# Optimization experiments

Hardware: AMD Instinct MI355X
Metric: run time of the kernel (lower is better)

## Reference

```python
import jax, jax.numpy as jnp
import numpy as np
from jax import lax

DRUG_LEN = 150
PROT_LEN = 1000
CHAR_DIM = 64
CONV = 40
C4 = CONV * 4  # 160
PROT_OUT = PROT_LEN - (4 - 1) - (8 - 1) - (12 - 1)  # 979


def conv1d(x, w, b):
    # x: (B, Cin, L), w: (Cout, Cin, K) -> (B, Cout, L-K+1), VALID
    y = lax.conv_general_dilated(x, w, window_strides=(1,), padding='VALID',
                                 dimension_numbers=('NCH', 'OIH', 'NCH'))
    return y + b[None, :, None]


def setup_inputs() -> dict:
    key = jax.random.key(0)
    ks = jax.random.split(key, 24)
    B = 4
    drug = jax.random.normal(ks[0], (B, DRUG_LEN, C4), dtype=jnp.float32)
    num_atoms = jax.random.randint(ks[1], (B,), 1, DRUG_LEN + 1)
    protein = jax.random.randint(ks[2], (B, PROT_LEN), 0, 26)

    def lin(k, dout, din, scale=None):
        s = scale if scale is not None else 1.0 / np.sqrt(din)
        kw, kb = jax.random.split(k)
        W = jax.random.uniform(kw, (dout, din), jnp.float32, -s, s)
        b = jax.random.uniform(kb, (dout,), jnp.float32, -s, s)
        return W, b

    protein_embed = jax.random.normal(ks[3], (26, CHAR_DIM), dtype=jnp.float32)
    protein_embed = protein_embed.at[0].set(0.0)  # padding_idx=0

    def conv_w(k, cout, cin, ksz):
        s = 1.0 / np.sqrt(cin * ksz)
        kw, kb = jax.random.split(k)
        w = jax.random.uniform(kw, (cout, cin, ksz), jnp.float32, -s, s)
        b = jax.random.uniform(kb, (cout,), jnp.float32, -s, s)
        return w, b

    w1, b1 = conv_w(ks[4], CONV, CHAR_DIM, 4)
    w2, b2 = conv_w(ks[5], CONV * 2, CONV, 8)
    w3, b3 = conv_w(ks[6], C4, CONV * 2, 12)
    Wd, bd = lin(ks[7], C4, C4)
    Wp, bp = lin(ks[8], C4, C4)
    Watt, batt = lin(ks[9], C4, C4)
    W1, bf1 = lin(ks[10], 1024, C4 * 2)
    W2, bf2 = lin(ks[11], 1024, 1024)
    W3, bf3 = lin(ks[12], 512, 1024)
    Wo, bo = lin(ks[13], 2, 512)
    return dict(drug=drug, num_atoms=num_atoms, protein=protein,
                protein_embed=protein_embed, w1=w1, b1=b1, w2=w2, b2=b2,
                w3=w3, b3=b3, Wd=Wd, bd=bd, Wp=Wp, bp=bp, Watt=Watt,
                batt=batt, W1=W1, bf1=bf1, W2=W2, bf2=bf2, W3=W3, bf3=bf3,
                Wo=Wo, bo=bo)


def _forward(drug, num_atoms, protein, protein_embed, w1, b1, w2, b2, w3, b3,
             Wd, bd, Wp, bp, Watt, batt, W1, bf1, W2, bf2, W3, bf3, Wo, bo):
    relu = jax.nn.relu
    drugConv = jnp.transpose(drug, (0, 2, 1))                 # (B,160,150)
    pe = jnp.transpose(protein_embed[protein], (0, 2, 1))     # (B,64,1000)
    h = relu(conv1d(pe, w1, b1))
    h = relu(conv1d(h, w2, b2))
    proteinConv = relu(conv1d(h, w3, b3))                     # (B,160,979)

    drug_att = drug @ Wd.T + bd                               # (B,150,160)
    dmask = (jnp.arange(DRUG_LEN)[None, :] < num_atoms[:, None])
    drug_att = drug_att * dmask[:, :, None]
    protein_att = jnp.transpose(proteinConv, (0, 2, 1)) @ Wp.T + bp  # (B,979,160)
    pmask = (protein > 0)[:, :PROT_OUT]
    protein_att = protein_att * pmask[:, :, None]

    # Broadcast outer-sum + relu; Linear commutes with mean (affine), so apply
    # attention_layer after reducing, identical math to Linear-then-mean.
    R = relu(drug_att[:, :, None, :] + protein_att[:, None, :, :])  # (B,150,979,160)
    Cmean = jnp.mean(R, axis=2)  # (B,150,160)
    Pmean = jnp.mean(R, axis=1)  # (B,979,160)
    Compound_atte = jax.nn.sigmoid(Cmean @ Watt.T + batt)  # (B,150,160)
    Protein_atte = jax.nn.sigmoid(Pmean @ Watt.T + batt)   # (B,979,160)

    drugConv = drugConv * (0.5 + jnp.transpose(Compound_atte, (0, 2, 1)))
    proteinConv = proteinConv * (0.5 + jnp.transpose(Protein_atte, (0, 2, 1)))
    d = jnp.max(drugConv, axis=2)      # (B,160) max-pool over full length
    p = jnp.max(proteinConv, axis=2)   # (B,160)
    pair = jnp.concatenate([d, p], axis=1)  # (B,320)

    lrelu = lambda x: jax.nn.leaky_relu(x, 0.01)
    f1 = lrelu(pair @ W1.T + bf1)
    f2 = lrelu(f1 @ W2.T + bf2)
    f3 = lrelu(f2 @ W3.T + bf3)
    return f3 @ Wo.T + bo  # (B,2)


def reference(drug, num_atoms, protein, protein_embed, w1, b1, w2, b2, w3, b3,
              Wd, bd, Wp, bp, Watt, batt, W1, bf1, W2, bf2, W3, bf3, Wo, bo):
    return _forward(drug, num_atoms, protein, protein_embed, w1, b1, w2, b2,
                    w3, b3, Wd, bd, Wp, bp, Watt, batt, W1, bf1, W2, bf2,
                    W3, bf3, Wo, bo)
```

## Files before the change

kernel.cpp:

```cpp
#include <hip/hip_runtime.h>
#include <math.h>

#define BB 4
#define DL 150
#define PL 1000
#define CD 64
#define NC1 40
#define NC2 80
#define NC3 160
#define L1O 997
#define L2O 990
#define L3O 979
#define L1P 1000
#define L2P 992
#define L3P 980
#define DLP 152
#define PLP 984
#define JP 992
#define NINF (-1e30f)

typedef __attribute__((ext_vector_type(8))) short bf16x8;
typedef __attribute__((ext_vector_type(4))) float f32x4;

__device__ __forceinline__ float relu_(float x){ return fmaxf(x, 0.f); }
__device__ __forceinline__ float lrelu_(float x){ return x > 0.f ? x : 0.01f * x; }

__device__ __forceinline__ unsigned fenc(float x){
  unsigned u = __float_as_uint(x);
  return (u & 0x80000000u) ? ~u : (u | 0x80000000u);
}
__device__ __forceinline__ float fdec(unsigned u){
  return __uint_as_float((u & 0x80000000u) ? (u & 0x7fffffffu) : ~u);
}
__device__ __forceinline__ float4 relu4_(float4 v){
  v.x = fmaxf(v.x, 0.f); v.y = fmaxf(v.y, 0.f);
  v.z = fmaxf(v.z, 0.f); v.w = fmaxf(v.w, 0.f);
  return v;
}
__device__ __forceinline__ unsigned short bf16_(float x){
  unsigned u = __float_as_uint(x);
  unsigned r = (u + 0x7FFFu + ((u >> 16) & 1u)) >> 16;
  return (unsigned short)r;
}

__device__ __forceinline__ f32x4 mfma_k160(const unsigned short* __restrict__ Wb,
                                           const unsigned short* __restrict__ Xb,
                                           int co0, int j0, int lane){
  int col = lane & 15, g = lane >> 4;
  f32x4 acc = {0.f, 0.f, 0.f, 0.f};
  const unsigned short* wr = Wb + (size_t)(co0 + col) * 160 + g * 8;
  const unsigned short* xr = Xb + (size_t)(j0 + col) * 160 + g * 8;
  #pragma unroll
  for (int k0 = 0; k0 < 5; k0++){
    bf16x8 av = *(const bf16x8*)(wr + k0 * 32);
    bf16x8 bv = *(const bf16x8*)(xr + k0 * 32);
    acc = __builtin_amdgcn_mfma_f32_16x16x32_bf16(av, bv, acc, 0, 0, 0);
  }
  return acc;
}

__global__ __launch_bounds__(256) void k_prep(const float* __restrict__ emb,
                       const float* __restrict__ w1, float* __restrict__ projG,
                       const float* __restrict__ w3, unsigned short* __restrict__ w3r,
                       const float* __restrict__ Wp, unsigned short* __restrict__ Wpb,
                       const float* __restrict__ Watt, unsigned short* __restrict__ Wattb){
  int blk = blockIdx.x;
  if (blk < 17){
    int e = blk * 256 + threadIdx.x;
    if (e >= 26 * 160) return;
    int tok = e / 160, rem = e % 160, k = rem / 40, co = rem % 40;
    float a = 0.f;
    const float* er = emb + tok * CD;
    const float* wr = w1 + co * (CD * 4) + k;
    #pragma unroll 8
    for (int ci = 0; ci < CD; ci++) a = fmaf(er[ci], wr[ci * 4], a);
    projG[tok * 161 + k * 40 + co] = a;
    return;
  }
  if (blk < 737){
    int e = (blk - 17) * 256 + threadIdx.x;
    if (e >= 12 * 160 * 96) return;
    int kk = e / (160 * 96); int r = e % (160 * 96);
    int co = r / 96, ci = r % 96;
    float v = (ci < NC2) ? w3[(size_t)co * 960 + ci * 12 + kk] : 0.f;
    w3r[e] = bf16_(v);
    return;
  }
  if (blk < 837){
    int e = (blk - 737) * 256 + threadIdx.x;
    if (e < 160 * 160) Wpb[e] = bf16_(Wp[e]);
    return;
  }
  int e = (blk - 837) * 256 + threadIdx.x;
  if (e < 160 * 160) Wattb[e] = bf16_(Watt[e]);
}

__global__ __launch_bounds__(256) void k_conv1(const int* __restrict__ prot,
                        const float* __restrict__ projG, const float* __restrict__ b1,
                        float* __restrict__ h1){
  __shared__ float sp[26 * 161];
  int b = blockIdx.x / 80;
  int t = (blockIdx.x % 80) * 256 + threadIdx.x;
  for (int k = threadIdx.x; k < 26 * 161; k += 256) sp[k] = projG[k];
  __syncthreads();
  int p = t & 1023, co2 = t >> 10;
  if (p >= L1O) return;
  const int* pr = prot + b * PL + p;
  int t0 = pr[0], t1 = pr[1], t2 = pr[2], t3 = pr[3];
  #pragma unroll
  for (int c = 0; c < 2; c++){
    int co = co2 * 2 + c;
    float a = b1[co] + sp[t0 * 161 + co] + sp[t1 * 161 + 40 + co]
            + sp[t2 * 161 + 80 + co] + sp[t3 * 161 + 120 + co];
    h1[(size_t)(b * NC1 + co) * L1P + p] = relu_(a);
  }
}

#define C2XW 44
#define C2WP 324
__global__ __launch_bounds__(128) void k_c2(const float* __restrict__ h1,
                        const float* __restrict__ w, const float* __restrict__ bias,
                        float* __restrict__ h2){
  __shared__ float xs[NC1 * C2XW];
  __shared__ float wl[16 * C2WP];
  int blk = blockIdx.x;
  int pt = blk % 31; int t = blk / 31;
  int cog = t % 5; int b = t / 5;
  int co0 = cog * 16, pblk = pt * 32;
  int tid = threadIdx.x;
  const float* xb = h1 + (size_t)(b * NC1) * L1P + pblk;
  for (int i = tid; i < 440; i += 128){
    int r = i / 11, c = i % 11;
    *(float4*)(&xs[r * C2XW + c * 4]) = *(const float4*)(xb + (size_t)r * L1P + c * 4);
  }
  for (int i = tid; i < 1280; i += 128){
    int cc = i / 80, c = i % 80;
    *(float4*)(&wl[cc * C2WP + c * 4]) =
        *(const float4*)(w + (size_t)(co0 + cc) * 320 + c * 4);
  }
  __syncthreads();
  int co_l = tid >> 3, pg = tid & 7, p0 = pg * 4;
  float acc[4] = {0,0,0,0};
  const float* wc = &wl[co_l * C2WP];
  #pragma unroll 2
  for (int ci = 0; ci < NC1; ci++){
    const float* xrow = &xs[ci * C2XW + p0];
    float xv[12];
    *(float4*)(&xv[0]) = *(const float4*)(xrow);
    *(float4*)(&xv[4]) = *(const float4*)(xrow + 4);
    *(float4*)(&xv[8]) = *(const float4*)(xrow + 8);
    float wk[8];
    *(float4*)(&wk[0]) = *(const float4*)(wc + ci * 8);
    *(float4*)(&wk[4]) = *(const float4*)(wc + ci * 8 + 4);
    #pragma unroll
    for (int k = 0; k < 8; k++){
      #pragma unroll
      for (int pp = 0; pp < 4; pp++)
        acc[pp] = fmaf(xv[pp + k], wk[k], acc[pp]);
    }
  }
  int co = co0 + co_l;
  float bv = bias[co];
  int pbase = pblk + p0;
  float* yr = h2 + (size_t)(b * NC2 + co) * L2P + pbase;
  if (pbase + 3 < L2O){
    float4 o; o.x = relu_(acc[0] + bv); o.y = relu_(acc[1] + bv);
    o.z = relu_(acc[2] + bv); o.w = relu_(acc[3] + bv);
    *(float4*)yr = o;
  } else {
    #pragma unroll
    for (int pp = 0; pp < 4; pp++)
      if (pbase + pp < L2O) yr[pp] = relu_(acc[pp] + bv);
  }
}

__global__ __launch_bounds__(256) void k_t2(const float* __restrict__ h2,
                        unsigned short* __restrict__ h2bT){
  __shared__ float tile[32][33];
  int blk = blockIdx.x;
  int pt = blk % 31; int t = blk / 31;
  int cit = t % 3; int b = t / 3;
  int ci0 = cit * 32, p0 = pt * 32;
  int r = threadIdx.x >> 5, c = threadIdx.x & 31;
  #pragma unroll
  for (int rr = 0; rr < 4; rr++){
    int ci = ci0 + r * 4 + rr;
    float v = (ci < NC2) ? h2[(size_t)(b * NC2 + ci) * L2P + p0 + c] : 0.f;
    tile[r * 4 + rr][c] = v;
  }
  __syncthreads();
  #pragma unroll
  for (int rr = 0; rr < 4; rr++){
    int prow = p0 + r * 4 + rr;
    h2bT[((size_t)b * 992 + prow) * 96 + ci0 + c] = bf16_(tile[c][r * 4 + rr]);
  }
}

__global__ __launch_bounds__(256) void k_c3m(const unsigned short* __restrict__ h2bT,
                        const unsigned short* __restrict__ w3r,
                        const float* __restrict__ bias, float* __restrict__ pconv,
                        unsigned short* __restrict__ pconvTb){
  int blk = blockIdx.x;
  int pt = blk % 16; int t = blk / 16;
  int cog = t % 10; int b = t / 10;
  int co0 = cog * 16;
  int wave = threadIdx.x >> 6, lane = threadIdx.x & 63;
  int col = lane & 15, g = lane >> 4;
  int p0 = pt * 64 + wave * 16;
  f32x4 acc = {0.f, 0.f, 0.f, 0.f};
  const unsigned short* wbase = w3r + (size_t)(co0 + col) * 96 + g * 8;
  const unsigned short* xbase = h2bT + (size_t)b * 992 * 96 + g * 8;
  int prow = p0 + col;
  for (int kk = 0; kk < 12; kk++){
    int rp = prow + kk; if (rp > 991) rp = 991;
    const unsigned short* xr = xbase + (size_t)rp * 96;
    const unsigned short* wr = wbase + (size_t)kk * (160 * 96);
    #pragma unroll
    for (int ks = 0; ks < 3; ks++){
      bf16x8 av = *(const bf16x8*)(wr + ks * 32);
      bf16x8 bv = *(const bf16x8*)(xr + ks * 32);
      acc = __builtin_amdgcn_mfma_f32_16x16x32_bf16(av, bv, acc, 0, 0, 0);
    }
  }
  if (p0 >= L3O) return;
  int p = p0 + col;
  if (p < L3O){
    unsigned short tb[4];
    #pragma unroll
    for (int r = 0; r < 4; r++){
      int co = co0 + g * 4 + r;
      float v = acc[r] + bias[co];
      pconv[(size_t)(b * NC3 + co) * L3P + p] = v;
      tb[r] = bf16_(relu_(v));
    }
    *(uint2*)(&pconvTb[((size_t)b * JP + p) * 160 + co0 + g * 4]) = *(uint2*)tb;
  }
}

__global__ __launch_bounds__(256) void k_patt(const float* __restrict__ drug,
                        const int* __restrict__ natoms,
                        const float* __restrict__ Wd, const float* __restrict__ bd,
                        float* __restrict__ dattT, unsigned* __restrict__ enc,
                        const unsigned short* __restrict__ pconvTb,
                        const int* __restrict__ prot,
                        const unsigned short* __restrict__ Wpb,
                        const float* __restrict__ bp, float* __restrict__ pattT){
  int blk = blockIdx.x;
  int tid = threadIdx.x;
  if (blk < 160){
    if (blk == 0){
      for (int k = tid; k < 2 * BB * NC3; k += 256) enc[k] = 0u;
    }
    int b = blk / 40, c0 = (blk % 40) * 4;
    int i = tid;
    if (i >= DL) return;
    const float4* xr = (const float4*)(drug + ((size_t)b * DL + i) * NC3);
    float4 a[4];
    #pragma unroll
    for (int cc = 0; cc < 4; cc++) a[cc] = make_float4(0.f, 0.f, 0.f, 0.f);
    for (int k4 = 0; k4 < 40; k4++){
      float4 xv = xr[k4];
      #pragma unroll
      for (int cc = 0; cc < 4; cc++){
        float4 wv = ((const float4*)(Wd + (size_t)(c0 + cc) * NC3))[k4];
        a[cc].x = fmaf(xv.x, wv.x, a[cc].x);
        a[cc].y = fmaf(xv.y, wv.y, a[cc].y);
        a[cc].z = fmaf(xv.z, wv.z, a[cc].z);
        a[cc].w = fmaf(xv.w, wv.w, a[cc].w);
      }
    }
    bool act = i < natoms[b];
    #pragma unroll
    for (int cc = 0; cc < 4; cc++){
      float r = act ? (a[cc].x + a[cc].y + a[cc].z + a[cc].w + bd[c0 + cc]) : 0.f;
      dattT[(size_t)(b * NC3 + c0 + cc) * DLP + i] = r;
    }
    return;
  }
  int q = blk - 160;
  int jt = q % 62, b = q / 62;
  int j0 = jt * 16;
  int wave = tid >> 6, lane = tid & 63;
  int col = lane & 15, g = lane >> 4;
  const unsigned short* Xb = pconvTb + (size_t)b * JP * 160;
  for (int ct = wave; ct < 10; ct += 4){
    int co0 = ct * 16;
    f32x4 acc = mfma_k160(Wpb, Xb, co0, j0, lane);
    int j = j0 + col;
    if (j < L3O){
      bool act = prot[b * PL + j] > 0;
      #pragma unroll
      for (int r = 0; r < 4; r++){
        int co = co0 + g * 4 + r;
        pattT[(size_t)(b * NC3 + co) * PLP + j] = act ? (acc[r] + bp[co]) : 0.f;
      }
    }
  }
}

__global__ __launch_bounds__(256) void k_means(const float* __restrict__ dattT,
                        const float* __restrict__ pattT,
                        float* __restrict__ cmeanT, float* __restrict__ pmeanT,
                        unsigned short* __restrict__ pmeanTb){
  __shared__ __align__(16) float sda[DLP];
  __shared__ __align__(16) float spa[PLP];
  __shared__ float scm[4][DLP];
  int b = blockIdx.x / NC3, c = blockIdx.x % NC3;
  int tid = threadIdx.x;
  const float4* dr = (const float4*)(dattT + (size_t)(b * NC3 + c) * DLP);
  const float4* pr = (const float4*)(pattT + (size_t)(b * NC3 + c) * PLP);
  if (tid < DLP / 4) *(float4*)(&sda[tid * 4]) = dr[tid];
  if (tid < PLP / 4) *(float4*)(&spa[tid * 4]) = pr[tid];
  __syncthreads();
  for (int t = tid; t < 600; t += 256){
    int i = t >> 2, qq = t & 3;
    int js = qq * 244;
    int je = (qq == 3) ? L3O : js + 244;
    float v = sda[i];
    float s0 = 0.f, s1 = 0.f, s2 = 0.f, s3 = 0.f;
    const float4* p4 = (const float4*)(spa + js);
    int n4 = (je - js) >> 2;
    for (int u = 0; u < n4; u++){
      float4 p = p4[u];
      s0 += relu_(v + p.x); s1 += relu_(v + p.y);
      s2 += relu_(v + p.z); s3 += relu_(v + p.w);
    }
    for (int j = js + n4 * 4; j < je; j++) s0 += relu_(v + spa[j]);
    scm[qq][i] = (s0 + s1) + (s2 + s3);
  }
  for (int j = tid; j < L3O; j += 256){
    float v = spa[j];
    float s0 = 0.f, s1 = 0.f, s2 = 0.f, s3 = 0.f;
    const float4* d4 = (const float4*)sda;
    #pragma unroll 4
    for (int u = 0; u < 37; u++){
      float4 d = d4[u];
      s0 += relu_(v + d.x); s1 += relu_(v + d.y);
      s2 += relu_(v + d.z); s3 += relu_(v + d.w);
    }
    s0 += relu_(v + sda[148]); s1 += relu_(v + sda[149]);
    float pm = ((s0 + s1) + (s2 + s3)) * (1.f / DL);
    pmeanT[(size_t)(b * NC3 + c) * PLP + j] = pm;
    pmeanTb[((size_t)b * JP + j) * 160 + c] = bf16_(pm);
  }
  __syncthreads();
  if (tid < DL){
    float s = (scm[0][tid] + scm[1][tid]) + (scm[2][tid] + scm[3][tid]);
    cmeanT[(size_t)(b * NC3 + c) * DLP + tid] = s * (1.f / L3O);
  }
}

__global__ __launch_bounds__(256) void k_atte(const float* __restrict__ cmeanT,
                        const unsigned short* __restrict__ pmeanTb,
                        const float* __restrict__ Watt,
                        const unsigned short* __restrict__ Wattb,
                        const float* __restrict__ batt,
                        const float* __restrict__ drug,
                        const float* __restrict__ pconv, unsigned* __restrict__ enc){
  int blk = blockIdx.x;
  int tid = threadIdx.x;
  if (blk < 160){
    __shared__ float sred[4][4];
    int b = blk / 40, c0 = (blk % 40) * 4;
    float m[4];
    #pragma unroll
    for (int cc = 0; cc < 4; cc++) m[cc] = NINF;
    int i = tid;
    if (i < DL){
      float acc[4];
      #pragma unroll
      for (int cc = 0; cc < 4; cc++) acc[cc] = batt[c0 + cc];
      const float* xc = cmeanT + (size_t)b * NC3 * DLP + i;
      const float* wr = Watt + (size_t)c0 * NC3;
      for (int cb = 0; cb < NC3; cb += 32){
        float xv[32];
        #pragma unroll
        for (int u = 0; u < 32; u++) xv[u] = xc[(size_t)(cb + u) * DLP];
        #pragma unroll
        for (int u = 0; u < 32; u++){
          #pragma unroll
          for (int cc = 0; cc < 4; cc++)
            acc[cc] = fmaf(xv[u], wr[(size_t)cc * NC3 + cb + u], acc[cc]);
        }
      }
      const float* gr = drug + ((size_t)b * DL + i) * NC3 + c0;
      #pragma unroll
      for (int cc = 0; cc < 4; cc++){
        float atte = 1.f / (1.f + expf(-acc[cc]));
        m[cc] = gr[cc] * (0.5f + atte);
      }
    }
    int wave = tid >> 6, lane = tid & 63;
    #pragma unroll
    for (int cc = 0; cc < 4; cc++){
      float v = m[cc];
      for (int off = 1; off < 64; off <<= 1) v = fmaxf(v, __shfl_xor(v, off, 64));
      if (lane == 0) sred[wave][cc] = v;
    }
    __syncthreads();
    if (tid < 4){
      float v = fmaxf(fmaxf(sred[0][tid], sred[1][tid]),
                      fmaxf(sred[2][tid], sred[3][tid]));
      atomicMax(&enc[b * NC3 + c0 + tid], fenc(v));
    }
    return;
  }
  int q = blk - 160;
  int jt = q % 62, b = q / 62;
  int j0 = jt * 16;
  int wave = tid >> 6, lane = tid & 63;
  int col = lane & 15, g = lane >> 4;
  const unsigned short* Xb = pmeanTb + (size_t)b * JP * 160;
  for (int ct = wave; ct < 10; ct += 4){
    int co0 = ct * 16;
    f32x4 acc = mfma_k160(Wattb, Xb, co0, j0, lane);
    int j = j0 + col;
    float m[4];
    #pragma unroll
    for (int r = 0; r < 4; r++){
      int co = co0 + g * 4 + r;
      if (j < L3O){
        float gate = 1.f / (1.f + expf(-(acc[r] + batt[co])));
        float pv = relu_(pconv[(size_t)(b * NC3 + co) * L3P + j]);
        m[r] = pv * (0.5f + gate);
      } else m[r] = NINF;
    }
    #pragma unroll
    for (int r = 0; r < 4; r++){
      #pragma unroll
      for (int off = 1; off < 16; off <<= 1)
        m[r] = fmaxf(m[r], __shfl_xor(m[r], off, 64));
    }
    if (col == 0){
      #pragma unroll
      for (int r = 0; r < 4; r++)
        atomicMax(&enc[BB * NC3 + b * NC3 + co0 + g * 4 + r], fenc(m[r]));
    }
  }
}

__global__ __launch_bounds__(256) void k_mlp1(const unsigned* __restrict__ enc,
                        const float* __restrict__ W1, const float* __restrict__ bf1,
                        float* __restrict__ f1){
  int b = blockIdx.x >> 6, og = blockIdx.x & 63;
  int o = og * 16 + (threadIdx.x >> 4);
  int q = threadIdx.x & 15;
  const float4* wr = (const float4*)(W1 + (size_t)o * 320);
  float4 a = make_float4(0.f, 0.f, 0.f, 0.f);
  #pragma unroll
  for (int mi = 0; mi < 5; mi++){
    int k4 = q + mi * 16;
    int k = k4 * 4;
    const unsigned* e = (k < 160) ? (enc + b * NC3 + k)
                                  : (enc + BB * NC3 + b * NC3 + (k - 160));
    float4 wv = wr[k4];
    a.x = fmaf(fdec(e[0]), wv.x, a.x);
    a.y = fmaf(fdec(e[1]), wv.y, a.y);
    a.z = fmaf(fdec(e[2]), wv.z, a.z);
    a.w = fmaf(fdec(e[3]), wv.w, a.w);
  }
  float r = a.x + a.y + a.z + a.w;
  r += __shfl_xor(r, 1, 64); r += __shfl_xor(r, 2, 64);
  r += __shfl_xor(r, 4, 64); r += __shfl_xor(r, 8, 64);
  if (q == 0) f1[b * 1024 + o] = lrelu_(r + bf1[o]);
}

__global__ __launch_bounds__(256) void k_mlp2(const float* __restrict__ x,
                        const float* __restrict__ W, const float* __restrict__ bias,
                        float* __restrict__ y){
  int b = blockIdx.x >> 6, og = blockIdx.x & 63;
  int o = og * 16 + (threadIdx.x >> 4);
  int q = threadIdx.x & 15;
  const float4* wr = (const float4*)(W + (size_t)o * 1024);
  const float4* xr = (const float4*)(x + b * 1024);
  float4 a = make_float4(0.f, 0.f, 0.f, 0.f);
  #pragma unroll
  for (int mi = 0; mi < 16; mi++){
    int k4 = q + mi * 16;
    float4 wv = wr[k4], xv = xr[k4];
    a.x = fmaf(xv.x, wv.x, a.x);
    a.y = fmaf(xv.y, wv.y, a.y);
    a.z = fmaf(xv.z, wv.z, a.z);
    a.w = fmaf(xv.w, wv.w, a.w);
  }
  float r = a.x + a.y + a.z + a.w;
  r += __shfl_xor(r, 1, 64); r += __shfl_xor(r, 2, 64);
  r += __shfl_xor(r, 4, 64); r += __shfl_xor(r, 8, 64);
  if (q == 0) y[b * 1024 + o] = lrelu_(r + bias[o]);
}

__global__ __launch_bounds__(256) void k_mlp3(const float* __restrict__ x,
                        const float* __restrict__ W, const float* __restrict__ bias,
                        float* __restrict__ y){
  int b = blockIdx.x >> 5, og = blockIdx.x & 31;
  int o = og * 16 + (threadIdx.x >> 4);
  int q = threadIdx.x & 15;
  const float4* wr = (const float4*)(W + (size_t)o * 1024);
  const float4* xr = (const float4*)(x + b * 1024);
  float4 a = make_float4(0.f, 0.f, 0.f, 0.f);
  #pragma unroll
  for (int mi = 0; mi < 16; mi++){
    int k4 = q + mi * 16;
    float4 wv = wr[k4], xv = xr[k4];
    a.x = fmaf(xv.x, wv.x, a.x);
    a.y = fmaf(xv.y, wv.y, a.y);
    a.z = fmaf(xv.z, wv.z, a.z);
    a.w = fmaf(xv.w, wv.w, a.w);
  }
  float r = a.x + a.y + a.z + a.w;
  r += __shfl_xor(r, 1, 64); r += __shfl_xor(r, 2, 64);
  r += __shfl_xor(r, 4, 64); r += __shfl_xor(r, 8, 64);
  if (q == 0) y[b * 512 + o] = lrelu_(r + bias[o]);
}

__global__ void k_mlp4(const float* __restrict__ f3, const float* __restrict__ Wo,
                       const float* __restrict__ bo, float* __restrict__ out){
  int tid = threadIdx.x;
  int g = tid >> 5, lane = tid & 31;
  int b = g >> 1, o = g & 1;
  const float4* xr = (const float4*)(f3 + b * 512);
  const float4* wr = (const float4*)(Wo + o * 512);
  float4 a = make_float4(0.f, 0.f, 0.f, 0.f);
  #pragma unroll
  for (int mI = 0; mI < 4; mI++){
    int k4 = lane + mI * 32;
    float4 xv = xr[k4], wv = wr[k4];
    a.x = fmaf(xv.x, wv.x, a.x);
    a.y = fmaf(xv.y, wv.y, a.y);
    a.z = fmaf(xv.z, wv.z, a.z);
    a.w = fmaf(xv.w, wv.w, a.w);
  }
  float r = a.x + a.y + a.z + a.w;
  for (int off = 16; off; off >>= 1) r += __shfl_xor(r, off, 64);
  if (lane == 0) out[b * 2 + o] = r + bo[o];
}

extern "C" void kernel_launch(void* const* d_in, const int* in_sizes, int n_in,
                              void* d_out, int out_size, void* d_ws, size_t ws_size,
                              hipStream_t stream) {
  const float* drug  = (const float*)d_in[0];
  const int*   natoms= (const int*)d_in[1];
  const int*   prot  = (const int*)d_in[2];
  const float* emb   = (const float*)d_in[3];
  const float* w1    = (const float*)d_in[4];
  const float* b1    = (const float*)d_in[5];
  const float* w2    = (const float*)d_in[6];
  const float* b2    = (const float*)d_in[7];
  const float* w3    = (const float*)d_in[8];
  const float* b3    = (const float*)d_in[9];
  const float* Wd    = (const float*)d_in[10];
  const float* bd    = (const float*)d_in[11];
  const float* Wp    = (const float*)d_in[12];
  const float* bp    = (const float*)d_in[13];
  const float* Watt  = (const float*)d_in[14];
  const float* batt  = (const float*)d_in[15];
  const float* W1    = (const float*)d_in[16];
  const float* bf1   = (const float*)d_in[17];
  const float* W2    = (const float*)d_in[18];
  const float* bf2   = (const float*)d_in[19];
  const float* W3    = (const float*)d_in[20];
  const float* bf3   = (const float*)d_in[21];
  const float* Wo    = (const float*)d_in[22];
  const float* bo    = (const float*)d_in[23];
  float* out = (float*)d_out;

  float* ws = (float*)d_ws;
  float* h1     = ws;
  float* cmeanT = ws;
  float* f1     = ws + 97280;
  float* f2     = ws + 101376;
  float* f3     = ws + 105472;
  float* h2     = ws + 160000;
  float* pconv  = ws + 477440;
  float* dattT  = ws + 1104640;
  float* pattT  = ws + 1201920;
  float* pmeanT = ws + 1831680;
  unsigned* enc = (unsigned*)(ws + 2461440);
  float* projG  = ws + 2461760;
  unsigned short* h2bT = (unsigned short*)(ws + 2466048);
  unsigned short* w3r  = (unsigned short*)(ws + 2656512);
  unsigned short* pconvTb = (unsigned short*)(ws + 2748672);
  unsigned short* pmeanTb = (unsigned short*)(ws + 3066112);
  unsigned short* Wpb   = (unsigned short*)(ws + 3383552);
  unsigned short* Wattb = (unsigned short*)(ws + 3396352);

  k_prep  <<<937, 256, 0, stream>>>(emb, w1, projG, w3, w3r, Wp, Wpb, Watt, Wattb);
  k_conv1 <<<BB * 80, 256, 0, stream>>>(prot, projG, b1, h1);
  k_c2    <<<620, 128, 0, stream>>>(h1, w2, b2, h2);
  k_t2    <<<372, 256, 0, stream>>>(h2, h2bT);
  k_c3m   <<<640, 256, 0, stream>>>(h2bT, w3r, b3, pconv, pconvTb);
  k_patt  <<<408, 256, 0, stream>>>(drug, natoms, Wd, bd, dattT, enc,
                                    pconvTb, prot, Wpb, bp, pattT);
  k_means <<<BB * NC3, 256, 0, stream>>>(dattT, pattT, cmeanT, pmeanT, pmeanTb);
  k_atte  <<<408, 256, 0, stream>>>(cmeanT, pmeanTb, Watt, Wattb, batt, drug,
                                    pconv, enc);
  k_mlp1  <<<256, 256, 0, stream>>>(enc, W1, bf1, f1);
  k_mlp2  <<<256, 256, 0, stream>>>(f1, W2, bf2, f2);
  k_mlp3  <<<128, 256, 0, stream>>>(f2, W3, bf3, f3);
  k_mlp4  <<<1, 256, 0, stream>>>(f3, Wo, bo, out);
}
```

Baseline: 106.2 us.

## Move conv2, drug linear and compound attention onto bf16 MFMA

Conv1 now writes a transposed bf16 activation, and conv2 becomes an MFMA kernel that writes the bf16 transposed layout conv3 consumes directly. This removes the separate transpose kernel and the fp32 intermediate. The drug projection and compound-side attention linear also switch from scalar fp32 FMA loops to MFMA, using new bf16 weight and drug copies made in the prep kernel. One launch and several fp32 round trips are removed, but more work shifts into the prep kernel and precision drops to bf16 on these paths.

```diff
diff --git a/kernel.cpp b/kernel.cpp
--- a/kernel.cpp
+++ b/kernel.cpp
@@ -11,8 +11,6 @@
 #define L1O 997
 #define L2O 990
 #define L3O 979
-#define L1P 1000
-#define L2P 992
 #define L3P 980
 #define DLP 152
 #define PLP 984
@@ -31,11 +29,6 @@
 }
 __device__ __forceinline__ float fdec(unsigned u){
   return __uint_as_float((u & 0x80000000u) ? (u & 0x7fffffffu) : ~u);
-}
-__device__ __forceinline__ float4 relu4_(float4 v){
-  v.x = fmaxf(v.x, 0.f); v.y = fmaxf(v.y, 0.f);
-  v.z = fmaxf(v.z, 0.f); v.w = fmaxf(v.w, 0.f);
-  return v;
 }
 __device__ __forceinline__ unsigned short bf16_(float x){
   unsigned u = __float_as_uint(x);
@@ -63,7 +56,10 @@
                        const float* __restrict__ w1, float* __restrict__ projG,
                        const float* __restrict__ w3, unsigned short* __restrict__ w3r,
                        const float* __restrict__ Wp, unsigned short* __restrict__ Wpb,
-                       const float* __restrict__ Watt, unsigned short* __restrict__ Wattb){
+                       const float* __restrict__ Watt, unsigned short* __restrict__ Wattb,
+                       const float* __restrict__ Wd, unsigned short* __restrict__ Wdb,
+                       const float* __restrict__ w2, unsigned short* __restrict__ w2r,
+                       const float* __restrict__ drug, unsigned short* __restrict__ drugb){
   int blk = blockIdx.x;
   if (blk < 17){
     int e = blk * 256 + threadIdx.x;
@@ -79,7 +75,6 @@
   }
   if (blk < 737){
     int e = (blk - 17) * 256 + threadIdx.x;
-    if (e >= 12 * 160 * 96) return;
     int kk = e / (160 * 96); int r = e % (160 * 96);
     int co = r / 96, ci = r % 96;
     float v = (ci < NC2) ? w3[(size_t)co * 960 + ci * 12 + kk] : 0.f;
@@ -88,111 +83,101 @@
   }
   if (blk < 837){
     int e = (blk - 737) * 256 + threadIdx.x;
-    if (e < 160 * 160) Wpb[e] = bf16_(Wp[e]);
-    return;
-  }
-  int e = (blk - 837) * 256 + threadIdx.x;
-  if (e < 160 * 160) Wattb[e] = bf16_(Watt[e]);
+    Wpb[e] = bf16_(Wp[e]);
+    return;
+  }
+  if (blk < 937){
+    int e = (blk - 837) * 256 + threadIdx.x;
+    Wattb[e] = bf16_(Watt[e]);
+    return;
+  }
+  if (blk < 1037){
+    int e = (blk - 937) * 256 + threadIdx.x;
+    Wdb[e] = bf16_(Wd[e]);
+    return;
+  }
+  if (blk < 1197){
+    int e = (blk - 1037) * 256 + threadIdx.x;
+    int kk = e / (80 * 64); int r = e % (80 * 64);
+    int co = r / 64, ci = r % 64;
+    float v = (ci < NC1) ? w2[(size_t)(co * NC1 + ci) * 8 + kk] : 0.f;
+    w2r[e] = bf16_(v);
+    return;
+  }
+  {
+    int e = (blk - 1197) * 256 + threadIdx.x;
+    int b = e / 25600; int r = e % 25600;
+    int i = r / 160, c = r % 160;
+    float v = (i < DL) ? drug[((size_t)b * DL + i) * 160 + c] : 0.f;
+    drugb[e] = bf16_(v);
+  }
 }
 
 __global__ __launch_bounds__(256) void k_conv1(const int* __restrict__ prot,
                         const float* __restrict__ projG, const float* __restrict__ b1,
-                        float* __restrict__ h1){
+                        unsigned short* __restrict__ h1bT){
   __shared__ float sp[26 * 161];
-  int b = blockIdx.x / 80;
-  int t = (blockIdx.x % 80) * 256 + threadIdx.x;
+  int b = blockIdx.x / 125;
+  int t = (blockIdx.x % 125) * 256 + threadIdx.x;
   for (int k = threadIdx.x; k < 26 * 161; k += 256) sp[k] = projG[k];
   __syncthreads();
-  int p = t & 1023, co2 = t >> 10;
-  if (p >= L1O) return;
-  const int* pr = prot + b * PL + p;
-  int t0 = pr[0], t1 = pr[1], t2 = pr[2], t3 = pr[3];
-  #pragma unroll
-  for (int c = 0; c < 2; c++){
-    int co = co2 * 2 + c;
-    float a = b1[co] + sp[t0 * 161 + co] + sp[t1 * 161 + 40 + co]
-            + sp[t2 * 161 + 80 + co] + sp[t3 * 161 + 120 + co];
-    h1[(size_t)(b * NC1 + co) * L1P + p] = relu_(a);
-  }
-}
-
-#define C2XW 44
-#define C2WP 324
-__global__ __launch_bounds__(128) void k_c2(const float* __restrict__ h1,
-                        const float* __restrict__ w, const float* __restrict__ bias,
-                        float* __restrict__ h2){
-  __shared__ float xs[NC1 * C2XW];
-  __shared__ float wl[16 * C2WP];
+  int ci = (t & 31) * 2, p = t >> 5;
+  float v0 = 0.f, v1 = 0.f;
+  if (p < L1O && ci < NC1){
+    const int* pr = prot + b * PL + p;
+    int t0 = pr[0], t1 = pr[1], t2 = pr[2], t3 = pr[3];
+    v0 = relu_(b1[ci] + sp[t0 * 161 + ci] + sp[t1 * 161 + 40 + ci]
+             + sp[t2 * 161 + 80 + ci] + sp[t3 * 161 + 120 + ci]);
+    int c1 = ci + 1;
+    v1 = relu_(b1[c1] + sp[t0 * 161 + c1] + sp[t1 * 161 + 40 + c1]
+             + sp[t2 * 161 + 80 + c1] + sp[t3 * 161 + 120 + c1]);
+  }
+  ushort2 o; o.x = bf16_(v0); o.y = bf16_(v1);
+  *(ushort2*)(&h1bT[((size_t)b * 1000 + p) * 64 + ci]) = o;
+}
+
+__global__ __launch_bounds__(256) void k_c2m(const unsigned short* __restrict__ h1bT,
+                        const unsigned short* __restrict__ w2r,
+                        const float* __restrict__ bias,
+                        unsigned short* __restrict__ h2bT){
   int blk = blockIdx.x;
-  int pt = blk % 31; int t = blk / 31;
+  int pt = blk % 16; int t = blk / 16;
   int cog = t % 5; int b = t / 5;
-  int co0 = cog * 16, pblk = pt * 32;
-  int tid = threadIdx.x;
-  const float* xb = h1 + (size_t)(b * NC1) * L1P + pblk;
-  for (int i = tid; i < 440; i += 128){
-    int r = i / 11, c = i % 11;
-    *(float4*)(&xs[r * C2XW + c * 4]) = *(const float4*)(xb + (size_t)r * L1P + c * 4);
-  }
-  for (int i = tid; i < 1280; i += 128){
-    int cc = i / 80, c = i % 80;
-    *(float4*)(&wl[cc * C2WP + c * 4]) =
-        *(const float4*)(w + (size_t)(co0 + cc) * 320 + c * 4);
-  }
-  __syncthreads();
-  int co_l = tid >> 3, pg = tid & 7, p0 = pg * 4;
-  float acc[4] = {0,0,0,0};
-  const float* wc = &wl[co_l * C2WP];
+  int co0 = cog * 16;
+  int wave = threadIdx.x >> 6, lane = threadIdx.x & 63;
+  int col = lane & 15, g = lane >> 4;
+  int p0 = pt * 64 + wave * 16;
+  if (p0 >= JP) return;
+  f32x4 acc = {0.f, 0.f, 0.f, 0.f};
+  const unsigned short* wbase = w2r + (size_t)(co0 + col) * 64 + g * 8;
+  const unsigned short* xbase = h1bT + (size_t)b * 1000 * 64 + g * 8;
+  int prow = p0 + col;
   #pragma unroll 2
-  for (int ci = 0; ci < NC1; ci++){
-    const float* xrow = &xs[ci * C2XW + p0];
-    float xv[12];
-    *(float4*)(&xv[0]) = *(const float4*)(xrow);
-    *(float4*)(&xv[4]) = *(const float4*)(xrow + 4);
-    *(float4*)(&xv[8]) = *(const float4*)(xrow + 8);
-    float wk[8];
-    *(float4*)(&wk[0]) = *(const float4*)(wc + ci * 8);
-    *(float4*)(&wk[4]) = *(const float4*)(wc + ci * 8 + 4);
-    #pragma unroll
-    for (int k = 0; k < 8; k++){
-      #pragma unroll
-      for (int pp = 0; pp < 4; pp++)
-        acc[pp] = fmaf(xv[pp + k], wk[k], acc[pp]);
-    }
-  }
-  int co = co0 + co_l;
-  float bv = bias[co];
-  int pbase = pblk + p0;
-  float* yr = h2 + (size_t)(b * NC2 + co) * L2P + pbase;
-  if (pbase + 3 < L2O){
-    float4 o; o.x = relu_(acc[0] + bv); o.y = relu_(acc[1] + bv);
-    o.z = relu_(acc[2] + bv); o.w = relu_(acc[3] + bv);
-    *(float4*)yr = o;
-  } else {
-    #pragma unroll
-    for (int pp = 0; pp < 4; pp++)
-      if (pbase + pp < L2O) yr[pp] = relu_(acc[pp] + bv);
-  }
-}
-
-__global__ __launch_bounds__(256) void k_t2(const float* __restrict__ h2,
-                        unsigned short* __restrict__ h2bT){
-  __shared__ float tile[32][33];
-  int blk = blockIdx.x;
-  int pt = blk % 31; int t = blk / 31;
-  int cit = t % 3; int b = t / 3;
-  int ci0 = cit * 32, p0 = pt * 32;
-  int r = threadIdx.x >> 5, c = threadIdx.x & 31;
-  #pragma unroll
-  for (int rr = 0; rr < 4; rr++){
-    int ci = ci0 + r * 4 + rr;
-    float v = (ci < NC2) ? h2[(size_t)(b * NC2 + ci) * L2P + p0 + c] : 0.f;
-    tile[r * 4 + rr][c] = v;
-  }
-  __syncthreads();
-  #pragma unroll
-  for (int rr = 0; rr < 4; rr++){
-    int prow = p0 + r * 4 + rr;
-    h2bT[((size_t)b * 992 + prow) * 96 + ci0 + c] = bf16_(tile[c][r * 4 + rr]);
+  for (int kk = 0; kk < 8; kk++){
+    int rp = prow + kk; if (rp > 999) rp = 999;
+    const unsigned short* xr = xbase + (size_t)rp * 64;
+    const unsigned short* wr = wbase + (size_t)kk * (80 * 64);
+    #pragma unroll
+    for (int ks = 0; ks < 2; ks++){
+      bf16x8 av = *(const bf16x8*)(wr + ks * 32);
+      bf16x8 bv = *(const bf16x8*)(xr + ks * 32);
+      acc = __builtin_amdgcn_mfma_f32_16x16x32_bf16(av, bv, acc, 0, 0, 0);
+    }
+  }
+  int p = p0 + col;
+  if (p < JP){
+    unsigned short tb[4];
+    bool live = p < L2O;
+    #pragma unroll
+    for (int r = 0; r < 4; r++){
+      int co = co0 + g * 4 + r;
+      tb[r] = live ? bf16_(relu_(acc[r] + bias[co])) : (unsigned short)0;
+    }
+    *(uint2*)(&h2bT[((size_t)b * JP + p) * 96 + co0 + g * 4]) = *(uint2*)tb;
+    if (cog == 4){
+      uint2 z = {0u, 0u};
+      *(uint2*)(&h2bT[((size_t)b * JP + p) * 96 + 80 + g * 4]) = z;
+    }
   }
 }
 
@@ -209,7 +194,7 @@
   int p0 = pt * 64 + wave * 16;
   f32x4 acc = {0.f, 0.f, 0.f, 0.f};
   const unsigned short* wbase = w3r + (size_t)(co0 + col) * 96 + g * 8;
-  const unsigned short* xbase = h2bT + (size_t)b * 992 * 96 + g * 8;
+  const unsigned short* xbase = h2bT + (size_t)b * JP * 96 + g * 8;
   int prow = p0 + col;
   for (int kk = 0; kk < 12; kk++){
     int rp = prow + kk; if (rp > 991) rp = 991;
@@ -237,9 +222,10 @@
   }
 }
 
-__global__ __launch_bounds__(256) void k_patt(const float* __restrict__ drug,
+__global__ __launch_bounds__(256) void k_pattm(const unsigned short* __restrict__ drugb,
                         const int* __restrict__ natoms,
-                        const float* __restrict__ Wd, const float* __restrict__ bd,
+                        const unsigned short* __restrict__ Wdb,
+                        const float* __restrict__ bd,
                         float* __restrict__ dattT, unsigned* __restrict__ enc,
                         const unsigned short* __restrict__ pconvTb,
                         const int* __restrict__ prot,
@@ -247,41 +233,33 @@
                         const float* __restrict__ bp, float* __restrict__ pattT){
   int blk = blockIdx.x;
   int tid = threadIdx.x;
-  if (blk < 160){
+  int wave = tid >> 6, lane = tid & 63;
+  int col = lane & 15, g = lane >> 4;
+  if (blk < 40){
     if (blk == 0){
       for (int k = tid; k < 2 * BB * NC3; k += 256) enc[k] = 0u;
     }
-    int b = blk / 40, c0 = (blk % 40) * 4;
-    int i = tid;
-    if (i >= DL) return;
-    const float4* xr = (const float4*)(drug + ((size_t)b * DL + i) * NC3);
-    float4 a[4];
-    #pragma unroll
-    for (int cc = 0; cc < 4; cc++) a[cc] = make_float4(0.f, 0.f, 0.f, 0.f);
-    for (int k4 = 0; k4 < 40; k4++){
-      float4 xv = xr[k4];
-      #pragma unroll
-      for (int cc = 0; cc < 4; cc++){
-        float4 wv = ((const float4*)(Wd + (size_t)(c0 + cc) * NC3))[k4];
-        a[cc].x = fmaf(xv.x, wv.x, a[cc].x);
-        a[cc].y = fmaf(xv.y, wv.y, a[cc].y);
-        a[cc].z = fmaf(xv.z, wv.z, a[cc].z);
-        a[cc].w = fmaf(xv.w, wv.w, a[cc].w);
+    int b = blk / 10, it = blk % 10;
+    int i0 = it * 16;
+    const unsigned short* Xb = drugb + (size_t)b * 160 * 160;
+    for (int ct = wave; ct < 10; ct += 4){
+      int co0 = ct * 16;
+      f32x4 acc = mfma_k160(Wdb, Xb, co0, i0, lane);
+      int i = i0 + col;
+      if (i < DL){
+        bool act = i < natoms[b];
+        #pragma unroll
+        for (int r = 0; r < 4; r++){
+          int co = co0 + g * 4 + r;
+          dattT[(size_t)(b * NC3 + co) * DLP + i] = act ? (acc[r] + bd[co]) : 0.f;
+        }
       }
     }
-    bool act = i < natoms[b];
-    #pragma unroll
-    for (int cc = 0; cc < 4; cc++){
-      float r = act ? (a[cc].x + a[cc].y + a[cc].z + a[cc].w + bd[c0 + cc]) : 0.f;
-      dattT[(size_t)(b * NC3 + c0 + cc) * DLP + i] = r;
-    }
-    return;
-  }
-  int q = blk - 160;
+    return;
+  }
+  int q = blk - 40;
   int jt = q % 62, b = q / 62;
   int j0 = jt * 16;
-  int wave = tid >> 6, lane = tid & 63;
-  int col = lane & 15, g = lane >> 4;
   const unsigned short* Xb = pconvTb + (size_t)b * JP * 160;
   for (int ct = wave; ct < 10; ct += 4){
     int co0 = ct * 16;
@@ -300,7 +278,7 @@
 
 __global__ __launch_bounds__(256) void k_means(const float* __restrict__ dattT,
                         const float* __restrict__ pattT,
-                        float* __restrict__ cmeanT, float* __restrict__ pmeanT,
+                        unsigned short* __restrict__ cmeanTb,
                         unsigned short* __restrict__ pmeanTb){
   __shared__ __align__(16) float sda[DLP];
   __shared__ __align__(16) float spa[PLP];
@@ -340,76 +318,64 @@
     }
     s0 += relu_(v + sda[148]); s1 += relu_(v + sda[149]);
     float pm = ((s0 + s1) + (s2 + s3)) * (1.f / DL);
-    pmeanT[(size_t)(b * NC3 + c) * PLP + j] = pm;
     pmeanTb[((size_t)b * JP + j) * 160 + c] = bf16_(pm);
   }
   __syncthreads();
-  if (tid < DL){
-    float s = (scm[0][tid] + scm[1][tid]) + (scm[2][tid] + scm[3][tid]);
-    cmeanT[(size_t)(b * NC3 + c) * DLP + tid] = s * (1.f / L3O);
-  }
-}
-
-__global__ __launch_bounds__(256) void k_atte(const float* __restrict__ cmeanT,
+  if (tid < 160){
+    float s = 0.f;
+    if (tid < DL)
+      s = ((scm[0][tid] + scm[1][tid]) + (scm[2][tid] + scm[3][tid])) * (1.f / L3O);
+    cmeanTb[((size_t)b * 160 + tid) * 160 + c] = bf16_(s);
+  }
+}
+
+__global__ __launch_bounds__(256) void k_attem(const unsigned short* __restrict__ cmeanTb,
                         const unsigned short* __restrict__ pmeanTb,
-                        const float* __restrict__ Watt,
                         const unsigned short* __restrict__ Wattb,
                         const float* __restrict__ batt,
                         const float* __restrict__ drug,
                         const float* __restrict__ pconv, unsigned* __restrict__ enc){
   int blk = blockIdx.x;
   int tid = threadIdx.x;
-  if (blk < 160){
-    __shared__ float sred[4][4];
-    int b = blk / 40, c0 = (blk % 40) * 4;
+  int wave = tid >> 6, lane = tid & 63;
+  int col = lane & 15, g = lane >> 4;
+  if (blk < 40){
+    int b = blk / 10, cot = blk % 10;
+    int co0 = cot * 16;
+    const unsigned short* Xb = cmeanTb + (size_t)b * 160 * 160;
     float m[4];
     #pragma unroll
-    for (int cc = 0; cc < 4; cc++) m[cc] = NINF;
-    int i = tid;
-    if (i < DL){
-      float acc[4];
-      #pragma unroll
-      for (int cc = 0; cc < 4; cc++) acc[cc] = batt[c0 + cc];
-      const float* xc = cmeanT + (size_t)b * NC3 * DLP + i;
-      const float* wr = Watt + (size_t)c0 * NC3;
-      for (int cb = 0; cb < NC3; cb += 32){
-        float xv[32];
+    for (int r = 0; r < 4; r++) m[r] = NINF;
+    for (int it = wave; it < 10; it += 4){
+      int i0 = it * 16;
+      f32x4 acc = mfma_k160(Wattb, Xb, co0, i0, lane);
+      int i = i0 + col;
+      if (i < DL){
         #pragma unroll
-        for (int u = 0; u < 32; u++) xv[u] = xc[(size_t)(cb + u) * DLP];
-        #pragma unroll
-        for (int u = 0; u < 32; u++){
-          #pragma unroll
-          for (int cc = 0; cc < 4; cc++)
-            acc[cc] = fmaf(xv[u], wr[(size_t)cc * NC3 + cb + u], acc[cc]);
+        for (int r = 0; r < 4; r++){
+          int co = co0 + g * 4 + r;
+          float gate = 1.f / (1.f + expf(-(acc[r] + batt[co])));
+          float val = drug[((size_t)b * DL + i) * 160 + co] * (0.5f + gate);
+          m[r] = fmaxf(m[r], val);
         }
       }
-      const float* gr = drug + ((size_t)b * DL + i) * NC3 + c0;
+    }
+    #pragma unroll
+    for (int r = 0; r < 4; r++){
       #pragma unroll
-      for (int cc = 0; cc < 4; cc++){
-        float atte = 1.f / (1.f + expf(-acc[cc]));
-        m[cc] = gr[cc] * (0.5f + atte);
-      }
-    }
-    int wave = tid >> 6, lane = tid & 63;
-    #pragma unroll
-    for (int cc = 0; cc < 4; cc++){
-      float v = m[cc];
-      for (int off = 1; off < 64; off <<= 1) v = fmaxf(v, __shfl_xor(v, off, 64));
-      if (lane == 0) sred[wave][cc] = v;
-    }
-    __syncthreads();
-    if (tid < 4){
-      float v = fmaxf(fmaxf(sred[0][tid], sred[1][tid]),
-                      fmaxf(sred[2][tid], sred[3][tid]));
-      atomicMax(&enc[b * NC3 + c0 + tid], fenc(v));
-    }
-    return;
-  }
-  int q = blk - 160;
+      for (int off = 1; off < 16; off <<= 1)
+        m[r] = fmaxf(m[r], __shfl_xor(m[r], off, 64));
+    }
+    if (col == 0){
+      #pragma unroll
+      for (int r = 0; r < 4; r++)
+        atomicMax(&enc[b * NC3 + co0 + g * 4 + r], fenc(m[r]));
+    }
+    return;
+  }
+  int q = blk - 40;
   int jt = q % 62, b = q / 62;
   int j0 = jt * 16;
-  int wave = tid >> 6, lane = tid & 63;
-  int col = lane & 15, g = lane >> 4;
   const unsigned short* Xb = pmeanTb + (size_t)b * JP * 160;
   for (int ct = wave; ct < 10; ct += 4){
     int co0 = ct * 16;
@@ -565,34 +531,35 @@
   float* out = (float*)d_out;
 
   float* ws = (float*)d_ws;
-  float* h1     = ws;
-  float* cmeanT = ws;
-  float* f1     = ws + 97280;
-  float* f2     = ws + 101376;
-  float* f3     = ws + 105472;
-  float* h2     = ws + 160000;
-  float* pconv  = ws + 477440;
-  float* dattT  = ws + 1104640;
-  float* pattT  = ws + 1201920;
-  float* pmeanT = ws + 1831680;
-  unsigned* enc = (unsigned*)(ws + 2461440);
-  float* projG  = ws + 2461760;
-  unsigned short* h2bT = (unsigned short*)(ws + 2466048);
-  unsigned short* w3r  = (unsigned short*)(ws + 2656512);
-  unsigned short* pconvTb = (unsigned short*)(ws + 2748672);
-  unsigned short* pmeanTb = (unsigned short*)(ws + 3066112);
-  unsigned short* Wpb   = (unsigned short*)(ws + 3383552);
-  unsigned short* Wattb = (unsigned short*)(ws + 3396352);
-
-  k_prep  <<<937, 256, 0, stream>>>(emb, w1, projG, w3, w3r, Wp, Wpb, Watt, Wattb);
-  k_conv1 <<<BB * 80, 256, 0, stream>>>(prot, projG, b1, h1);
-  k_c2    <<<620, 128, 0, stream>>>(h1, w2, b2, h2);
-  k_t2    <<<372, 256, 0, stream>>>(h2, h2bT);
+  float* f1     = ws;
+  float* f2     = ws + 4096;
+  float* f3     = ws + 8192;
+  float* dattT  = ws + 10240;
+  float* pattT  = ws + 107520;
+  float* pconv  = ws + 737280;
+  unsigned* enc = (unsigned*)(ws + 1364480);
+  float* projG  = ws + 1364864;
+  unsigned short* h1bT    = (unsigned short*)(ws + 1369088);
+  unsigned short* w2r     = (unsigned short*)(ws + 1497088);
+  unsigned short* h2bT    = (unsigned short*)(ws + 1517568);
+  unsigned short* w3r     = (unsigned short*)(ws + 1708032);
+  unsigned short* pconvTb = (unsigned short*)(ws + 1800192);
+  unsigned short* pmeanTb = (unsigned short*)(ws + 2117632);
+  unsigned short* cmeanTb = (unsigned short*)(ws + 2435072);
+  unsigned short* drugb   = (unsigned short*)(ws + 2486272);
+  unsigned short* Wpb     = (unsigned short*)(ws + 2537472);
+  unsigned short* Wattb   = (unsigned short*)(ws + 2550272);
+  unsigned short* Wdb     = (unsigned short*)(ws + 2563072);
+
+  k_prep  <<<1597, 256, 0, stream>>>(emb, w1, projG, w3, w3r, Wp, Wpb,
+                                     Watt, Wattb, Wd, Wdb, w2, w2r, drug, drugb);
+  k_conv1 <<<500, 256, 0, stream>>>(prot, projG, b1, h1bT);
+  k_c2m   <<<320, 256, 0, stream>>>(h1bT, w2r, b2, h2bT);
   k_c3m   <<<640, 256, 0, stream>>>(h2bT, w3r, b3, pconv, pconvTb);
-  k_patt  <<<408, 256, 0, stream>>>(drug, natoms, Wd, bd, dattT, enc,
+  k_pattm <<<288, 256, 0, stream>>>(drugb, natoms, Wdb, bd, dattT, enc,
                                     pconvTb, prot, Wpb, bp, pattT);
-  k_means <<<BB * NC3, 256, 0, stream>>>(dattT, pattT, cmeanT, pmeanT, pmeanTb);
-  k_atte  <<<408, 256, 0, stream>>>(cmeanT, pmeanTb, Watt, Wattb, batt, drug,
+  k_means <<<BB * NC3, 256, 0, stream>>>(dattT, pattT, cmeanTb, pmeanTb);
+  k_attem <<<288, 256, 0, stream>>>(cmeanTb, pmeanTb, Wattb, batt, drug,
                                     pconv, enc);
   k_mlp1  <<<256, 256, 0, stream>>>(enc, W1, bf1, f1);
   k_mlp2  <<<256, 256, 0, stream>>>(f1, W2, bf2, f2);
```

Result: faster. 98.47 us (median of 3 runs) (-7.2%).
